# Performance work log

Hardware: AMD Instinct MI355X
Metric: run time of the kernel (lower is better)

## Reference

```python
import jax, jax.numpy as jnp
import numpy as np

HIDDEN_DIM = 64
VOCAB_SIZE = 64
ENTROPY_THRESH = 2.5
SCALE = 1.0 / np.sqrt(HIDDEN_DIM)


def setup_inputs() -> dict:
    key = jax.random.key(0)
    ks = jax.random.split(key, 16)
    B, L, M = 1024, 2048, 256
    H = HIDDEN_DIM
    seq = jax.random.randint(ks[0], (B, L), 0, VOCAB_SIZE, dtype=jnp.int64 if jax.config.jax_enable_x64 else jnp.int32)
    memory = jax.random.normal(ks[1], (B, M, H), dtype=jnp.float32)
    s = 0.05
    params = {
        'embed':  jax.random.normal(ks[2], (VOCAB_SIZE, H)) * s,
        'w_ih':   jax.random.normal(ks[3], (3 * H, 2 * H)) * s,
        'w_hh':   jax.random.normal(ks[4], (3 * H, H)) * s,
        'b_ih':   jax.random.normal(ks[5], (3 * H,)) * s,
        'b_hh':   jax.random.normal(ks[6], (3 * H,)) * s,
        'wq':     jax.random.normal(ks[7], (H, H)) * s,
        'bq':     jax.random.normal(ks[8], (H,)) * s,
        'wk':     jax.random.normal(ks[9], (H, H)) * s,
        'bk':     jax.random.normal(ks[10], (H,)) * s,
        'wv':     jax.random.normal(ks[11], (H, H)) * s,
        'bv':     jax.random.normal(ks[12], (H,)) * s,
        'head_w': jax.random.normal(ks[13], (VOCAB_SIZE, H)) * s,
        'head_b': jax.random.normal(ks[14], (VOCAB_SIZE,)) * s,
    }
    return dict(seq=seq, memory=memory, **params)


def _attention(h, memory, wq, bq, wk, bk, wv, bv):
    # h: [B,H], memory: [B,M,H]
    q = h @ wq.T + bq                                  # [B,H]
    k = jnp.einsum('bmh,oh->bmo', memory, wk) + bk     # [B,M,H]
    v = jnp.einsum('bmh,oh->bmo', memory, wv) + bv     # [B,M,H]
    scores = jnp.einsum('bh,bmh->bm', q, k) * SCALE    # [B,M]
    w = jax.nn.softmax(scores, axis=-1)
    return jnp.einsum('bm,bmh->bh', w, v)              # [B,H]


def _forward(seq, memory, embed, w_ih, w_hh, b_ih, b_hh,
             wq, bq, wk, bk, wv, bv, head_w, head_b):
    B, L = seq.shape
    H = HIDDEN_DIM
    h0 = jnp.zeros((B, H), dtype=memory.dtype)
    r0 = jnp.zeros((B, H), dtype=memory.dtype)

    def step(carry, seq_t):
        h, retrieved, read_count = carry
        x_t = embed[seq_t]                              # [B,H] gather
        inp = jnp.concatenate([x_t, retrieved], axis=-1)  # [B,2H]
        gi = inp @ w_ih.T + b_ih                        # [B,3H]
        gh = h @ w_hh.T + b_hh                          # [B,3H]
        i_r, i_z, i_n = jnp.split(gi, 3, axis=-1)
        h_r, h_z, h_n = jnp.split(gh, 3, axis=-1)
        r = jax.nn.sigmoid(i_r + h_r)
        z = jax.nn.sigmoid(i_z + h_z)
        n = jnp.tanh(i_n + r * h_n)
        h_new = (1.0 - z) * n + z * h
        # entropy gate (no_grad in original)
        logits_t = jax.lax.stop_gradient(h_new @ head_w.T + head_b)
        probs = jax.nn.softmax(logits_t, axis=-1)
        entropy = -(probs * jnp.log(probs + 1e-8)).sum(-1)  # [B]
        cond = entropy.mean() > ENTROPY_THRESH              # scalar bool
        att = _attention(h_new, memory, wq, bq, wk, bk, wv, bv)
        retrieved_new = jnp.where(cond, att, jnp.zeros_like(att))
        return (h_new, retrieved_new, read_count + cond.astype(jnp.int32)), None

    (h, _, read_count), _ = jax.lax.scan(step, (h0, r0, jnp.int32(0)), seq.T)
    logits = h @ head_w.T + head_b
    read_rate = read_count.astype(jnp.float32) / L
    return logits, read_rate


def reference(seq, memory, embed, w_ih, w_hh, b_ih, b_hh,
              wq, bq, wk, bk, wv, bv, head_w, head_b):
    return _forward(seq, memory, embed, w_ih, w_hh, b_ih, b_hh,
                    wq, bq, wk, bk, wv, bv, head_w, head_b)
```

## Files before the change

### kernel.cpp

```cpp
#include <hip/hip_runtime.h>
#include <stdint.h>

#define HD       64
#define MM       256
#define BB       1024
#define LL       2048
#define SCALE_   0.125f
#define GATE_SUM (2560ull << 20)
#define M30      0x3FFFFFFFull
#define M48      0xFFFFFFFFFFFFull
#define SPIN_FAR 16384
#define SPIN_LDS (1 << 20)

#define WS_SLOTS 0
#define WS_MIRR  8192
#define WS_WPA   12288
#define WS_WPB   36864
#define WS_G     61440
#define WS_HWT2  86016
#define WS_W2    102400
#define WS_D     118784
#define WS_E     119040
#define WS_F     119296

#define LD_WPA   0
#define LD_WPB   24576
#define LD_G     49152
#define LD_HWT2  73728
#define LD_DYN   90112
#define DYN_STRIDE 5120
#define DY_GI    0
#define DY_GH    1536
#define DY_H0A   2304
#define DY_H1A   2560
#define DY_H0B   2816
#define DY_H1B   3072
#define DY_NUM   3328
#define DY_WEA   3840
#define DY_WEB   4352
#define DY_SEH   4864
#define LD_MISC  110592

#define P0_W2P   0
#define P0_WVT2  8192
#define P0_D     16384
#define P0_E     16640
#define P0_F     16896
#define P0_MC    17408
#define MC_BYTES 16640

#define LDS_BYTES 150528

__device__ __forceinline__ unsigned bf16r(float x) {
  unsigned u = __float_as_uint(x);
  return (u + 0x7fffu + ((u >> 16) & 1u)) >> 16;
}
__device__ __forceinline__ unsigned pack2(float a, float b) {
  return bf16r(a) | (bf16r(b) << 16);
}
__device__ __forceinline__ float lo16(unsigned u) { return __uint_as_float(u << 16); }
__device__ __forceinline__ float hi16(unsigned u) { return __uint_as_float(u & 0xffff0000u); }

#define WAVE_FENCE() asm volatile("s_waitcnt lgkmcnt(0)" ::: "memory")

extern "C" __global__ void reactive_pre(
    const float* __restrict__ embed, const float* __restrict__ w_ih,
    const float* __restrict__ w_hh,  const float* __restrict__ b_ih,
    const float* __restrict__ wq,    const float* __restrict__ bq,
    const float* __restrict__ wk,    const float* __restrict__ bk,
    const float* __restrict__ head_w, unsigned char* __restrict__ ws)
{
  const int tid = threadIdx.x;

  unsigned* wpa = (unsigned*)(ws + WS_WPA);
  unsigned* wpb = (unsigned*)(ws + WS_WPB);
  for (int i = tid; i < 6144; i += 1024) {
    int q = i / 192, row = i % 192;
    wpa[i] = pack2(w_ih[row * 128 + 64 + 2 * q], w_ih[row * 128 + 64 + 2 * q + 1]);
    wpb[i] = pack2(w_hh[row * 64 + 2 * q],       w_hh[row * 64 + 2 * q + 1]);
  }
  unsigned* gp = (unsigned*)(ws + WS_G);
  for (int i = tid; i < 64 * 96; i += 1024) {
    int v = i / 96, u = i % 96;
    int j0 = 2 * u, j1 = j0 + 1;
    float g0 = b_ih[j0], g1 = b_ih[j1];
    for (int h = 0; h < 64; ++h) {
      float ev = embed[v * 64 + h];
      g0 = fmaf(ev, w_ih[j0 * 128 + h], g0);
      g1 = fmaf(ev, w_ih[j1 * 128 + h], g1);
    }
    gp[i] = pack2(g0, g1);
  }
  float2* hwt2 = (float2*)(ws + WS_HWT2);
  for (int i = tid; i < 2048; i += 1024) {
    int hp = i >> 6, o = i & 63;
    hwt2[i] = make_float2(head_w[o * 64 + 2 * hp], head_w[o * 64 + 2 * hp + 1]);
  }
  float* w2 = (float*)(ws + WS_W2);
  for (int i = tid; i < 4096; i += 1024) {
    int h2 = i >> 6, h = i & 63;
    float a = 0.f;
    for (int o = 0; o < 64; ++o) a = fmaf(wk[o * 64 + h2], wq[o * 64 + h], a);
    w2[i] = a;
  }
  if (tid < 64) {
    float a = 0.f, b2 = 0.f;
    for (int o = 0; o < 64; ++o) a  = fmaf(bk[o], wq[o * 64 + tid], a);
    for (int o = 0; o < 64; ++o) b2 = fmaf(bq[o], wk[o * 64 + tid], b2);
    ((float*)(ws + WS_D))[tid] = a;
    ((float*)(ws + WS_E))[tid] = b2;
  }
  if (tid == 0) {
    float a = 0.f;
    for (int o = 0; o < 64; ++o) a = fmaf(bq[o], bk[o], a);
    *(float*)(ws + WS_F) = a;
  }
}

extern "C" __global__ void __launch_bounds__(512, 2)
reactive_main(const int* __restrict__ seq, const float* __restrict__ memory,
              const float* __restrict__ wvp, const float* __restrict__ bvp,
              const float* __restrict__ b_hh, const float* __restrict__ head_w,
              const float* __restrict__ head_b, unsigned char* __restrict__ ws,
              float* __restrict__ out)
{
  extern __shared__ __align__(16) unsigned char lds[];
  const int tid     = threadIdx.x;
  const int wv      = tid >> 6;
  const int lane    = tid & 63;
  const int half    = wv >> 2;
  const int b_local = wv & 3;
  const int b       = (int)blockIdx.x * 4 + b_local;
  const int grp     = (int)blockIdx.x & 63;
  const bool isA    = (half == 0);
  const bool isRes  = (blockIdx.x == 0) && (wv == 0);

  unsigned kp[2][32];
  unsigned vt[64];
  float    cm[2];

  {
    unsigned* w2p  = (unsigned*)(lds + P0_W2P);
    unsigned* wvt2 = (unsigned*)(lds + P0_WVT2);
    float* pD = (float*)(lds + P0_D);
    float* pE = (float*)(lds + P0_E);
    float* pF = (float*)(lds + P0_F);
    const float* wsW2 = (const float*)(ws + WS_W2);
    for (int i = tid; i < 2048; i += 512) {
      int h2 = i >> 5, hp = i & 31;
      w2p[i] = pack2(wsW2[h2 * 64 + 2 * hp], wsW2[h2 * 64 + 2 * hp + 1]);
    }
    for (int i = tid; i < 2048; i += 512) {
      int h2p = i >> 6, l = i & 63;
      wvt2[i] = pack2(wvp[l * 64 + 2 * h2p], wvp[l * 64 + 2 * h2p + 1]);
    }
    if (tid < 64) { pD[tid] = ((const float*)(ws + WS_D))[tid];
                    pE[tid] = ((const float*)(ws + WS_E))[tid]; }
    if (tid == 0) pF[0] = *(const float*)(ws + WS_F);
    __syncthreads();

    float* mc = (float*)(lds + P0_MC + wv * MC_BYTES);
    const float bvl   = bvp[lane];
    const float fscal = pF[0];
    const float* memb = memory + ((size_t)b * MM + (size_t)half * 128) * HD;

    for (int g = 0; g < 2; ++g) {
      WAVE_FENCE();
#pragma unroll 4
      for (int r = 0; r < 64; ++r)
        mc[r * 65 + lane] = memb[(size_t)(g * 64 + r) * HD + lane];
      WAVE_FENCE();

      float acc[64];
#pragma unroll
      for (int h = 0; h < 64; ++h) acc[h] = pD[h];
      float cacc = fscal;
      for (int h2 = 0; h2 < 64; ++h2) {
        float mv = mc[lane * 65 + h2];
        cacc = fmaf(mv, pE[h2], cacc);
        const unsigned* wrow = w2p + h2 * 32;
#pragma unroll
        for (int hp = 0; hp < 32; ++hp) {
          unsigned u = wrow[hp];
          acc[2 * hp]     = fmaf(mv, lo16(u), acc[2 * hp]);
          acc[2 * hp + 1] = fmaf(mv, hi16(u), acc[2 * hp + 1]);
        }
      }
      cm[g] = cacc;
#pragma unroll
      for (int u = 0; u < 32; ++u) kp[g][u] = pack2(acc[2 * u], acc[2 * u + 1]);

      for (int rp = 0; rp < 32; ++rp) {
        float a0 = bvl, a1 = bvl;
#pragma unroll
        for (int hq = 0; hq < 32; ++hq) {
          unsigned w = wvt2[hq * 64 + lane];
          float wl = lo16(w), wh = hi16(w);
          const float2 m0 = *(const float2*)&mc[(2 * rp) * 65 + 2 * hq];
          const float2 m1 = *(const float2*)&mc[(2 * rp + 1) * 65 + 2 * hq];
          a0 = fmaf(m0.x, wl, a0); a0 = fmaf(m0.y, wh, a0);
          a1 = fmaf(m1.x, wl, a1); a1 = fmaf(m1.y, wh, a1);
        }
        vt[32 * g + rp] = pack2(a0, a1);
      }
    }
    __syncthreads();
  }

  {
    const float4* s1 = (const float4*)(ws + WS_WPA);   float4* d1 = (float4*)(lds + LD_WPA);
    for (int i = tid; i < 1536; i += 512) d1[i] = s1[i];
    const float4* s2 = (const float4*)(ws + WS_WPB);   float4* d2 = (float4*)(lds + LD_WPB);
    for (int i = tid; i < 1536; i += 512) d2[i] = s2[i];
    const float4* s3 = (const float4*)(ws + WS_G);     float4* d3 = (float4*)(lds + LD_G);
    for (int i = tid; i < 1536; i += 512) d3[i] = s3[i];
    const float4* s4 = (const float4*)(ws + WS_HWT2);  float4* d4 = (float4*)(lds + LD_HWT2);
    for (int i = tid; i < 1024; i += 512) d4[i] = s4[i];
    float* dz = (float*)(lds + LD_DYN);
    for (int i = tid; i < 4 * DYN_STRIDE / 4; i += 512) dz[i] = 0.f;
    if (tid < 5) ((unsigned*)(lds + LD_MISC))[tid] = 0u;
    __syncthreads();
    if (tid < 4) {
      float* se = (float*)(lds + LD_DYN + tid * DYN_STRIDE + DY_SEH);
      se[0] = 1.f; se[1] = 1.f;
    }
    __syncthreads();
  }

  const unsigned* sWPA = (const unsigned*)(lds + LD_WPA);
  const unsigned* sWPB = (const unsigned*)(lds + LD_WPB);
  const unsigned* sG   = (const unsigned*)(lds + LD_G);
  const float2*   sHW2 = (const float2*)(lds + LD_HWT2);
  unsigned char* dynp = lds + LD_DYN + b_local * DYN_STRIDE;
  float* sGI  = (float*)(dynp + DY_GI);
  float* sGH  = (float*)(dynp + DY_GH);
  float* sH0me = (float*)(dynp + (isA ? DY_H0A : DY_H0B));
  float* sH1me = (float*)(dynp + (isA ? DY_H1A : DY_H1B));
  float* sNUM = (float*)(dynp + DY_NUM);
  float* sWE  = (float*)(dynp + (isA ? DY_WEA : DY_WEB));
  float* sSEH = (float*)(dynp + DY_SEH);
  unsigned long long* sBEC = (unsigned long long*)(lds + LD_MISC);
  volatile unsigned* sCONDW = (volatile unsigned*)(lds + LD_MISC + 16);
  unsigned long long* slots = (unsigned long long*)(ws + WS_SLOTS);
  unsigned long long* mirr  = (unsigned long long*)(ws + WS_MIRR);
  const unsigned long long* mline = mirr + (size_t)grp * 8;
  const int* seqb = seq + (size_t)b * LL;

  float h_reg = 0.f;
  float* hsel_last = sH0me;
  int res_t = 0, rcount = 0;
  unsigned condbits = 0;
  unsigned long long rpe0_0 = 0ull, rpe1_0 = 0ull;
  unsigned long long rpe0_1 = 0ull, rpe1_1 = 0ull;
  bool cprev = false;

  float bh_r = 0.f, bh_z = 0.f, bh_n = 0.f;
  if (!isA) { bh_r = b_hh[lane]; bh_z = b_hh[64 + lane]; bh_n = b_hh[128 + lane]; }
  const float hb_l = head_b[lane];

  float a_gr = 0.f, a_gz = 0.f, a_gn = 0.f, a_dr = 0.f, a_dz = 0.f, a_dn = 0.f;
  float b_hr = 0.f, b_hz = 0.f, b_hn = 0.f;

  for (int t = 0; t < LL; ++t) {
    if (isA) {
      float Se = sSEH[0] + sSEH[1];
      float rcpSe = 1.0f / Se;
      int token = seqb[t];
      float sr = 0.f, sz = 0.f, sn = 0.f;
#pragma unroll
      for (int q = 0; q < 32; ++q) {
        float2 n0 = *(const float2*)&sNUM[2 * q];
        float2 n1 = *(const float2*)&sNUM[64 + 2 * q];
        float a0 = n0.x + n1.x, a1 = n0.y + n1.y;
        unsigned ur = sWPA[q * 192 + lane];
        unsigned uz = sWPA[q * 192 + 64 + lane];
        unsigned un = sWPA[q * 192 + 128 + lane];
        sr = fmaf(a0, lo16(ur), sr); sr = fmaf(a1, hi16(ur), sr);
        sz = fmaf(a0, lo16(uz), sz); sz = fmaf(a1, hi16(uz), sz);
        sn = fmaf(a0, lo16(un), sn); sn = fmaf(a1, hi16(un), sn);
      }
      unsigned gp0 = sG[token * 96 +      (lane >> 1)];
      unsigned gp1 = sG[token * 96 + 32 + (lane >> 1)];
      unsigned gp2 = sG[token * 96 + 64 + (lane >> 1)];
      bool oddl = (lane & 1);
      a_gr = oddl ? hi16(gp0) : lo16(gp0);
      a_gz = oddl ? hi16(gp1) : lo16(gp1);
      a_gn = oddl ? hi16(gp2) : lo16(gp2);
      a_dr = rcpSe * sr; a_dz = rcpSe * sz; a_dn = rcpSe * sn;
      sGI[lane] = a_gr;        sGI[64 + lane] = a_gz;  sGI[128 + lane] = a_gn;
      sGI[192 + lane] = a_dr;  sGI[256 + lane] = a_dz; sGI[320 + lane] = a_dn;
    } else {
      float hr = bh_r, hz = bh_z, hn = bh_n;
      const float* hprev = hsel_last;
#pragma unroll
      for (int q = 0; q < 32; ++q) {
        float2 h01 = *(const float2*)&hprev[2 * q];
        unsigned ur = sWPB[q * 192 + lane];
        unsigned uz = sWPB[q * 192 + 64 + lane];
        unsigned un = sWPB[q * 192 + 128 + lane];
        hr = fmaf(h01.x, lo16(ur), hr); hr = fmaf(h01.y, hi16(ur), hr);
        hz = fmaf(h01.x, lo16(uz), hz); hz = fmaf(h01.y, hi16(uz), hz);
        hn = fmaf(h01.x, lo16(un), hn); hn = fmaf(h01.y, hi16(un), hn);
      }
      b_hr = hr; b_hz = hz; b_hn = hn;
      sGH[lane] = hr; sGH[64 + lane] = hz; sGH[128 + lane] = hn;
    }
    __syncthreads();

    float gi_r, gi_z, gi_n, da_r, da_z, da_n, gh_r, gh_z, gh_n;
    if (isA) {
      gh_r = sGH[lane]; gh_z = sGH[64 + lane]; gh_n = sGH[128 + lane];
      gi_r = a_gr; gi_z = a_gz; gi_n = a_gn; da_r = a_dr; da_z = a_dz; da_n = a_dn;
    } else {
      gi_r = sGI[lane];       gi_z = sGI[64 + lane];  gi_n = sGI[128 + lane];
      da_r = sGI[192 + lane]; da_z = sGI[256 + lane]; da_n = sGI[320 + lane];
      gh_r = b_hr; gh_z = b_hz; gh_n = b_hn;
    }
    float xr0 = gi_r + gh_r, xz0 = gi_z + gh_z;
    float rg0 = 1.f / (1.f + __expf(-xr0));
    float rg1 = 1.f / (1.f + __expf(-(xr0 + da_r)));
    float zg0 = 1.f / (1.f + __expf(-xz0));
    float zg1 = 1.f / (1.f + __expf(-(xz0 + da_z)));
    float na0 = fmaf(rg0, gh_n, gi_n);
    float na1 = fmaf(rg1, gh_n, gi_n + da_n);
    float ee0 = __expf(-2.f * na0), ee1 = __expf(-2.f * na1);
    float n0 = (1.f - ee0) / (1.f + ee0);
    float n1 = (1.f - ee1) / (1.f + ee1);
    float h0 = (1.f - zg0) * n0 + zg0 * h_reg;
    float h1 = (1.f - zg1) * n1 + zg1 * h_reg;
    sH0me[lane] = h0; sH1me[lane] = h1;
    WAVE_FENCE();

    {
      const float* hme = isA ? sH0me : sH1me;
      float lo = hb_l;
#pragma unroll
      for (int hp = 0; hp < 32; ++hp) {
        float2 h01 = *(const float2*)&hme[2 * hp];
        float2 w = sHW2[hp * 64 + lane];
        lo = fmaf(h01.x, w.x, lo); lo = fmaf(h01.y, w.y, lo);
      }
      float pu = __expf(lo);
      float Ss = pu;
#pragma unroll
      for (int off = 32; off; off >>= 1) Ss += __shfl_xor(Ss, off, 64);
      float pr = pu / Ss;
      float ent = pr * __logf(pr + 1e-8f);
#pragma unroll
      for (int off = 32; off; off >>= 1) ent += __shfl_xor(ent, off, 64);
      if (lane == 0) {
        float be = fmaxf(-ent, 0.f);
        unsigned long long fp = (unsigned long long)(unsigned)(be * 1048576.0f + 0.5f);
        unsigned long long add = (1ull << 60) | (isA ? fp : (fp << 30));
        unsigned long long old = atomicAdd(&sBEC[t & 1], add);
        if ((old >> 60) == 7ull) {
          unsigned long long tot = old + add;
          unsigned long long e0s = tot & M30;
          unsigned long long e1s = (tot >> 30) & M30;
          unsigned long long* line = slots + ((size_t)grp * 2 + (size_t)(t & 1)) * 8;
          __hip_atomic_fetch_add(line,     (1ull << 48) | e0s,
                                 __ATOMIC_RELAXED, __HIP_MEMORY_SCOPE_AGENT);
          __hip_atomic_fetch_add(line + 1, (1ull << 48) | e1s,
                                 __ATOMIC_RELAXED, __HIP_MEMORY_SCOPE_AGENT);
          sBEC[t & 1] = 0ull;
        }
      }
    }

    bool condp = false;
    if (t > 0) {
      if (isRes) {
        while (res_t < t) {
          int par = res_t & 1;
          unsigned long long* lp = slots + ((size_t)lane * 2 + (size_t)par) * 8;
          unsigned long long b0 = par ? rpe0_1 : rpe0_0;
          unsigned long long b1 = par ? rpe1_1 : rpe1_0;
          unsigned long long c0, c1;
          int guard = SPIN_FAR;
          for (;;) {
            c0 = __hip_atomic_load(lp,     __ATOMIC_RELAXED, __HIP_MEMORY_SCOPE_AGENT);
            c1 = __hip_atomic_load(lp + 1, __ATOMIC_RELAXED, __HIP_MEMORY_SCOPE_AGENT);
            bool ok = (((c0 - b0) >> 48) == 4ull) && (((c1 - b1) >> 48) == 4ull);
            if (__all(ok)) break;
            if (--guard <= 0) break;
            __builtin_amdgcn_s_sleep(1);
          }
          unsigned long long d = cprev ? ((c1 - b1) & M48) : ((c0 - b0) & M48);
          if (par) { rpe0_1 = c0; rpe1_1 = c1; } else { rpe0_0 = c0; rpe1_0 = c1; }
#pragma unroll
          for (int off = 32; off; off >>= 1) d += __shfl_xor(d, off, 64);
          bool c = d > GATE_SUM;
          cprev = c; rcount += c ? 1 : 0;
          condbits = (condbits << 1) | (c ? 1u : 0u);
          ++res_t;
          unsigned long long mv = ((unsigned long long)res_t << 32) | condbits;
          __hip_atomic_store(mirr + (size_t)lane * 8, mv,
                             __ATOMIC_RELAXED, __HIP_MEMORY_SCOPE_AGENT);
        }
        condp = cprev;
        if (lane == 0) *sCONDW = ((unsigned)(t + 1) << 1) | (condp ? 1u : 0u);
      } else if (wv == 0) {
        unsigned long long v;
        unsigned hi;
        int guard = SPIN_FAR;
        for (;;) {
          v = __hip_atomic_load(mline, __ATOMIC_RELAXED, __HIP_MEMORY_SCOPE_AGENT);
          hi = (unsigned)(v >> 32);
          if (hi >= (unsigned)t) break;
          if (--guard <= 0) break;
          __builtin_amdgcn_s_sleep(1);
        }
        condp = (hi >= (unsigned)t) ? (((v >> (hi - (unsigned)t)) & 1ull) != 0ull) : false;
        if (lane == 0) *sCONDW = ((unsigned)(t + 1) << 1) | (condp ? 1u : 0u);
      } else {
        unsigned cv;
        int guard = SPIN_LDS;
        for (;;) {
          cv = *sCONDW;
          if ((cv >> 1) == (unsigned)(t + 1)) break;
          if (--guard <= 0) break;
          __builtin_amdgcn_s_sleep(0);
        }
        condp = ((cv >> 1) == (unsigned)(t + 1)) ? ((cv & 1u) != 0u) : false;
      }
    }
    float h_new = condp ? h1 : h0;
    float* hsel = condp ? sH1me : sH0me;
    hsel_last = hsel;
    h_reg = h_new;

    float s0 = cm[0], s1 = cm[1];
#pragma unroll
    for (int hp = 0; hp < 32; ++hp) {
      float2 h01 = *(const float2*)&hsel[2 * hp];
      unsigned u0 = kp[0][hp], u1 = kp[1][hp];
      s0 = fmaf(h01.x, lo16(u0), s0); s0 = fmaf(h01.y, hi16(u0), s0);
      s1 = fmaf(h01.x, lo16(u1), s1); s1 = fmaf(h01.y, hi16(u1), s1);
    }
    float e0 = __expf(s0 * SCALE_), e1 = __expf(s1 * SCALE_);
    float seh = e0 + e1;
#pragma unroll
    for (int off = 32; off; off >>= 1) seh += __shfl_xor(seh, off, 64);
    sWE[lane] = e0; sWE[64 + lane] = e1;
    if (lane == 0) sSEH[half] = seh;
    WAVE_FENCE();

    float al = 0.f;
    const float4* w4 = (const float4*)sWE;
#pragma unroll
    for (int mp = 0; mp < 32; ++mp) {
      float4 wq4 = w4[mp];
      unsigned u0 = vt[2 * mp], u1 = vt[2 * mp + 1];
      al = fmaf(wq4.x, lo16(u0), al);
      al = fmaf(wq4.y, hi16(u0), al);
      al = fmaf(wq4.z, lo16(u1), al);
      al = fmaf(wq4.w, hi16(u1), al);
    }
    sNUM[half * 64 + lane] = al;
    __syncthreads();
  }

  if (isRes) {
    while (res_t < LL) {
      int par = res_t & 1;
      unsigned long long* lp = slots + ((size_t)lane * 2 + (size_t)par) * 8;
      unsigned long long b0 = par ? rpe0_1 : rpe0_0;
      unsigned long long b1 = par ? rpe1_1 : rpe1_0;
      unsigned long long c0, c1;
      int guard = SPIN_FAR;
      for (;;) {
        c0 = __hip_atomic_load(lp,     __ATOMIC_RELAXED, __HIP_MEMORY_SCOPE_AGENT);
        c1 = __hip_atomic_load(lp + 1, __ATOMIC_RELAXED, __HIP_MEMORY_SCOPE_AGENT);
        bool ok = (((c0 - b0) >> 48) == 4ull) && (((c1 - b1) >> 48) == 4ull);
        if (__all(ok)) break;
        if (--guard <= 0) break;
        __builtin_amdgcn_s_sleep(1);
      }
      unsigned long long d = cprev ? ((c1 - b1) & M48) : ((c0 - b0) & M48);
      if (par) { rpe0_1 = c0; rpe1_1 = c1; } else { rpe0_0 = c0; rpe1_0 = c1; }
#pragma unroll
      for (int off = 32; off; off >>= 1) d += __shfl_xor(d, off, 64);
      bool c = d > GATE_SUM;
      cprev = c; rcount += c ? 1 : 0;
      ++res_t;
    }
    if (lane == 0) out[BB * 64] = (float)rcount / (float)LL;
  }

  if (isA) {
    float lof = hb_l;
#pragma unroll 8
    for (int h = 0; h < 64; ++h) lof = fmaf(hsel_last[h], head_w[lane * 64 + h], lof);
    out[(size_t)b * 64 + lane] = lof;
  }
}

extern "C" void kernel_launch(void* const* d_in, const int* in_sizes, int n_in,
                              void* d_out, int out_size, void* d_ws, size_t ws_size,
                              hipStream_t stream)
{
  (void)in_sizes; (void)n_in; (void)out_size; (void)ws_size;
  const int*   seq    = (const int*)  d_in[0];
  const float* memory = (const float*)d_in[1];
  const float* embed  = (const float*)d_in[2];
  const float* w_ih   = (const float*)d_in[3];
  const float* w_hh   = (const float*)d_in[4];
  const float* b_ih   = (const float*)d_in[5];
  const float* b_hh   = (const float*)d_in[6];
  const float* wq     = (const float*)d_in[7];
  const float* bq     = (const float*)d_in[8];
  const float* wk     = (const float*)d_in[9];
  const float* bk     = (const float*)d_in[10];
  const float* wv     = (const float*)d_in[11];
  const float* bv     = (const float*)d_in[12];
  const float* head_w = (const float*)d_in[13];
  const float* head_b = (const float*)d_in[14];
  unsigned char* ws   = (unsigned char*)d_ws;
  float* out          = (float*)d_out;

  hipMemsetAsync(d_ws, 0, 12288, stream);

  hipLaunchKernelGGL(reactive_pre, dim3(1), dim3(1024), 0, stream,
                     embed, w_ih, w_hh, b_ih, wq, bq, wk, bk, head_w, ws);

  hipFuncSetAttribute((const void*)reactive_main,
                      hipFuncAttributeMaxDynamicSharedMemorySize, LDS_BYTES);
  hipLaunchKernelGGL(reactive_main, dim3(256), dim3(512), LDS_BYTES, stream,
                     seq, memory, wv, bv, b_hh, head_w, head_b, ws, out);
}
```

Baseline: 21.07 ms.

## Replace resolver-plus-mirror grid sync with per-block ring slots read by every block

Each block now writes its packed entropy sums, tagged with the step number, into a 4-deep ring of per-block slots in global memory, replacing atomic adds into grouped counters. Every block's wave 0 now reads all 256 slots and makes the gate decision itself, instead of waiting for one resolver wave to publish condition bits through a mirror line. This removes a serial hop (resolver to mirror to other blocks) from the per-step cross-block critical path. In exchange, every block polls all 256 slots each step, raising global memory traffic and contention, and the packed fields are narrowed to 25 bits per sum.

```diff
diff --git a/kernel.cpp b/kernel.cpp
--- a/kernel.cpp
+++ b/kernel.cpp
@@ -8,20 +8,19 @@
 #define SCALE_   0.125f
 #define GATE_SUM (2560ull << 20)
 #define M30      0x3FFFFFFFull
-#define M48      0xFFFFFFFFFFFFull
+#define M25      0x1FFFFFFull
 #define SPIN_FAR 16384
 #define SPIN_LDS (1 << 20)
 
-#define WS_SLOTS 0
-#define WS_MIRR  8192
-#define WS_WPA   12288
-#define WS_WPB   36864
-#define WS_G     61440
-#define WS_HWT2  86016
-#define WS_W2    102400
-#define WS_D     118784
-#define WS_E     119040
-#define WS_F     119296
+#define WS_RING  0
+#define WS_WPA   8192
+#define WS_WPB   32768
+#define WS_G     57344
+#define WS_HWT2  81920
+#define WS_W2    98304
+#define WS_D     114688
+#define WS_E     114944
+#define WS_F     115200
 
 #define LD_WPA   0
 #define LD_WPB   24576
@@ -131,9 +130,7 @@
   const int half    = wv >> 2;
   const int b_local = wv & 3;
   const int b       = (int)blockIdx.x * 4 + b_local;
-  const int grp     = (int)blockIdx.x & 63;
   const bool isA    = (half == 0);
-  const bool isRes  = (blockIdx.x == 0) && (wv == 0);
 
   unsigned kp[2][32];
   unsigned vt[64];
@@ -241,17 +238,12 @@
   float* sSEH = (float*)(dynp + DY_SEH);
   unsigned long long* sBEC = (unsigned long long*)(lds + LD_MISC);
   volatile unsigned* sCONDW = (volatile unsigned*)(lds + LD_MISC + 16);
-  unsigned long long* slots = (unsigned long long*)(ws + WS_SLOTS);
-  unsigned long long* mirr  = (unsigned long long*)(ws + WS_MIRR);
-  const unsigned long long* mline = mirr + (size_t)grp * 8;
+  unsigned long long* ring = (unsigned long long*)(ws + WS_RING);
   const int* seqb = seq + (size_t)b * LL;
 
   float h_reg = 0.f;
   float* hsel_last = sH0me;
   int res_t = 0, rcount = 0;
-  unsigned condbits = 0;
-  unsigned long long rpe0_0 = 0ull, rpe1_0 = 0ull;
-  unsigned long long rpe0_1 = 0ull, rpe1_1 = 0ull;
   bool cprev = false;
 
   float bh_r = 0.f, bh_z = 0.f, bh_n = 0.f;
@@ -357,11 +349,9 @@
           unsigned long long tot = old + add;
           unsigned long long e0s = tot & M30;
           unsigned long long e1s = (tot >> 30) & M30;
-          unsigned long long* line = slots + ((size_t)grp * 2 + (size_t)(t & 1)) * 8;
-          __hip_atomic_fetch_add(line,     (1ull << 48) | e0s,
-                                 __ATOMIC_RELAXED, __HIP_MEMORY_SCOPE_AGENT);
-          __hip_atomic_fetch_add(line + 1, (1ull << 48) | e1s,
-                                 __ATOMIC_RELAXED, __HIP_MEMORY_SCOPE_AGENT);
+          unsigned long long pk = ((unsigned long long)(t + 1) << 50) | (e1s << 25) | e0s;
+          __hip_atomic_store(ring + (((size_t)(t & 3)) << 8) + blockIdx.x, pk,
+                             __ATOMIC_RELAXED, __HIP_MEMORY_SCOPE_AGENT);
           sBEC[t & 1] = 0ull;
         }
       }
@@ -369,48 +359,35 @@
 
     bool condp = false;
     if (t > 0) {
-      if (isRes) {
+      if (wv == 0) {
         while (res_t < t) {
-          int par = res_t & 1;
-          unsigned long long* lp = slots + ((size_t)lane * 2 + (size_t)par) * 8;
-          unsigned long long b0 = par ? rpe0_1 : rpe0_0;
-          unsigned long long b1 = par ? rpe1_1 : rpe1_0;
-          unsigned long long c0, c1;
+          const unsigned long long* rb =
+              ring + (((size_t)(res_t & 3)) << 8) + 4 * lane;
+          unsigned long long want = (unsigned long long)(res_t + 1);
+          unsigned long long v0, v1, v2, v3;
           int guard = SPIN_FAR;
           for (;;) {
-            c0 = __hip_atomic_load(lp,     __ATOMIC_RELAXED, __HIP_MEMORY_SCOPE_AGENT);
-            c1 = __hip_atomic_load(lp + 1, __ATOMIC_RELAXED, __HIP_MEMORY_SCOPE_AGENT);
-            bool ok = (((c0 - b0) >> 48) == 4ull) && (((c1 - b1) >> 48) == 4ull);
+            v0 = __hip_atomic_load(rb + 0, __ATOMIC_RELAXED, __HIP_MEMORY_SCOPE_AGENT);
+            v1 = __hip_atomic_load(rb + 1, __ATOMIC_RELAXED, __HIP_MEMORY_SCOPE_AGENT);
+            v2 = __hip_atomic_load(rb + 2, __ATOMIC_RELAXED, __HIP_MEMORY_SCOPE_AGENT);
+            v3 = __hip_atomic_load(rb + 3, __ATOMIC_RELAXED, __HIP_MEMORY_SCOPE_AGENT);
+            bool ok = ((v0 >> 50) == want) && ((v1 >> 50) == want) &&
+                      ((v2 >> 50) == want) && ((v3 >> 50) == want);
             if (__all(ok)) break;
             if (--guard <= 0) break;
             __builtin_amdgcn_s_sleep(1);
           }
-          unsigned long long d = cprev ? ((c1 - b1) & M48) : ((c0 - b0) & M48);
-          if (par) { rpe0_1 = c0; rpe1_1 = c1; } else { rpe0_0 = c0; rpe1_0 = c1; }
+          unsigned long long d;
+          if (cprev) d = ((v0 >> 25) & M25) + ((v1 >> 25) & M25) +
+                         ((v2 >> 25) & M25) + ((v3 >> 25) & M25);
+          else       d = (v0 & M25) + (v1 & M25) + (v2 & M25) + (v3 & M25);
 #pragma unroll
           for (int off = 32; off; off >>= 1) d += __shfl_xor(d, off, 64);
           bool c = d > GATE_SUM;
           cprev = c; rcount += c ? 1 : 0;
-          condbits = (condbits << 1) | (c ? 1u : 0u);
           ++res_t;
-          unsigned long long mv = ((unsigned long long)res_t << 32) | condbits;
-          __hip_atomic_store(mirr + (size_t)lane * 8, mv,
-                             __ATOMIC_RELAXED, __HIP_MEMORY_SCOPE_AGENT);
         }
         condp = cprev;
-        if (lane == 0) *sCONDW = ((unsigned)(t + 1) << 1) | (condp ? 1u : 0u);
-      } else if (wv == 0) {
-        unsigned long long v;
-        unsigned hi;
-        int guard = SPIN_FAR;
-        for (;;) {
-          v = __hip_atomic_load(mline, __ATOMIC_RELAXED, __HIP_MEMORY_SCOPE_AGENT);
-          hi = (unsigned)(v >> 32);
-          if (hi >= (unsigned)t) break;
-          if (--guard <= 0) break;
-          __builtin_amdgcn_s_sleep(1);
-        }
-        condp = (hi >= (unsigned)t) ? (((v >> (hi - (unsigned)t)) & 1ull) != 0ull) : false;
         if (lane == 0) *sCONDW = ((unsigned)(t + 1) << 1) | (condp ? 1u : 0u);
       } else {
         unsigned cv;
@@ -460,24 +437,28 @@
     __syncthreads();
   }
 
-  if (isRes) {
+  if (blockIdx.x == 0 && wv == 0) {
     while (res_t < LL) {
-      int par = res_t & 1;
-      unsigned long long* lp = slots + ((size_t)lane * 2 + (size_t)par) * 8;
-      unsigned long long b0 = par ? rpe0_1 : rpe0_0;
-      unsigned long long b1 = par ? rpe1_1 : rpe1_0;
-      unsigned long long c0, c1;
+      const unsigned long long* rb =
+          ring + (((size_t)(res_t & 3)) << 8) + 4 * lane;
+      unsigned long long want = (unsigned long long)(res_t + 1);
+      unsigned long long v0, v1, v2, v3;
       int guard = SPIN_FAR;
       for (;;) {
-        c0 = __hip_atomic_load(lp,     __ATOMIC_RELAXED, __HIP_MEMORY_SCOPE_AGENT);
-        c1 = __hip_atomic_load(lp + 1, __ATOMIC_RELAXED, __HIP_MEMORY_SCOPE_AGENT);
-        bool ok = (((c0 - b0) >> 48) == 4ull) && (((c1 - b1) >> 48) == 4ull);
+        v0 = __hip_atomic_load(rb + 0, __ATOMIC_RELAXED, __HIP_MEMORY_SCOPE_AGENT);
+        v1 = __hip_atomic_load(rb + 1, __ATOMIC_RELAXED, __HIP_MEMORY_SCOPE_AGENT);
+        v2 = __hip_atomic_load(rb + 2, __ATOMIC_RELAXED, __HIP_MEMORY_SCOPE_AGENT);
+        v3 = __hip_atomic_load(rb + 3, __ATOMIC_RELAXED, __HIP_MEMORY_SCOPE_AGENT);
+        bool ok = ((v0 >> 50) == want) && ((v1 >> 50) == want) &&
+                  ((v2 >> 50) == want) && ((v3 >> 50) == want);
         if (__all(ok)) break;
         if (--guard <= 0) break;
         __builtin_amdgcn_s_sleep(1);
       }
-      unsigned long long d = cprev ? ((c1 - b1) & M48) : ((c0 - b0) & M48);
-      if (par) { rpe0_1 = c0; rpe1_1 = c1; } else { rpe0_0 = c0; rpe1_0 = c1; }
+      unsigned long long d;
+      if (cprev) d = ((v0 >> 25) & M25) + ((v1 >> 25) & M25) +
+                     ((v2 >> 25) & M25) + ((v3 >> 25) & M25);
+      else       d = (v0 & M25) + (v1 & M25) + (v2 & M25) + (v3 & M25);
 #pragma unroll
       for (int off = 32; off; off >>= 1) d += __shfl_xor(d, off, 64);
       bool c = d > GATE_SUM;
@@ -518,7 +499,7 @@
   unsigned char* ws   = (unsigned char*)d_ws;
   float* out          = (float*)d_out;
 
-  hipMemsetAsync(d_ws, 0, 12288, stream);
+  hipMemsetAsync(d_ws, 0, 8192, stream);
 
   hipLaunchKernelGGL(reactive_pre, dim3(1), dim3(1024), 0, stream,
                      embed, w_ih, w_hh, b_ih, wq, bq, wk, bk, head_w, ws);
```

New measurement: 21.56 ms. +2.3%, slower.
